# Kernel optimization log

Hardware: AMD Instinct MI355X
Metric: run time of the kernel (lower is better)

Reference implementation:

```python
import jax, jax.numpy as jnp
import numpy as np

N_HEAD = 16
D_MODEL = 1024
D_K = 64
D_V = 64
LN_EPS = 1e-5


def setup_inputs() -> dict:
    key = jax.random.key(0)
    ks = jax.random.split(key, 12)
    B, S = 4, 1024
    std_qkv = np.sqrt(2.0 / (D_MODEL + D_K)).astype(np.float32)
    inp = {
        "q": jax.random.normal(ks[0], (B, S, D_MODEL), jnp.float32),
        "k": jax.random.normal(ks[1], (B, S, D_MODEL), jnp.float32),
        "v": jax.random.normal(ks[2], (B, S, D_MODEL), jnp.float32),
        "Wq": jax.random.normal(ks[3], (N_HEAD * D_K, D_MODEL), jnp.float32) * std_qkv,
        "bq": jnp.zeros((N_HEAD * D_K,), jnp.float32),
        "Wk": jax.random.normal(ks[4], (N_HEAD * D_K, D_MODEL), jnp.float32) * std_qkv,
        "bk": jnp.zeros((N_HEAD * D_K,), jnp.float32),
        "Wv": jax.random.normal(ks[5], (N_HEAD * D_K, D_MODEL), jnp.float32) * std_qkv,
        "bv": jnp.zeros((N_HEAD * D_K,), jnp.float32),
        "Wfc": jax.random.normal(ks[6], (D_MODEL, N_HEAD * D_V), jnp.float32) * np.sqrt(2.0 / (D_MODEL + N_HEAD * D_V)).astype(np.float32),
        "bfc": jnp.zeros((D_MODEL,), jnp.float32),
        "gamma": jnp.ones((D_MODEL,), jnp.float32),
        "beta": jnp.zeros((D_MODEL,), jnp.float32),
    }
    return inp


def reference(q, k, v, Wq, bq, Wk, bk, Wv, bv, Wfc, bfc, gamma, beta):
    B, S, D = q.shape
    residual = q
    # projections -> [B, S, H, d] -> [B, H, S, d]
    qh = (q @ Wq.T + bq).reshape(B, S, N_HEAD, D_K).transpose(0, 2, 1, 3)
    kh = (k @ Wk.T + bk).reshape(B, S, N_HEAD, D_K).transpose(0, 2, 1, 3)
    vh = (v @ Wv.T + bv).reshape(B, S, N_HEAD, D_V).transpose(0, 2, 1, 3)
    # NOTE: faithful to source -- no 1/sqrt(d_k) scaling (temperature is None)
    scores = jnp.einsum('bhqd,bhkd->bhqk', qh, kh)  # [B, H, S, S]
    attn = jax.nn.softmax(scores, axis=-1)
    out = jnp.einsum('bhqk,bhkd->bhqd', attn, vh)  # [B, H, S, d_v]
    out = out.transpose(0, 2, 1, 3).reshape(B, S, N_HEAD * D_V)
    out = out @ Wfc.T + bfc  # dropout = identity at eval
    x = out + residual
    mu = jnp.mean(x, axis=-1, keepdims=True)
    var = jnp.var(x, axis=-1, keepdims=True)
    y = (x - mu) * jax.lax.rsqrt(var + LN_EPS) * gamma + beta
    # attn returned in source layout: (n_head*batch, S, S)
    attn_flat = attn.transpose(1, 0, 2, 3).reshape(N_HEAD * B, S, S)
    return (y, attn_flat)
```

## Files before the change

### kernel.cpp

```cpp
#include <hip/hip_runtime.h>
#include <stdint.h>

#define B_ 4
#define S_ 1024
#define D_ 1024
#define H_ 16
#define DK_ 64

typedef unsigned short u16;
typedef unsigned int   u32;
typedef short bf16x8 __attribute__((ext_vector_type(8)));
typedef float f32x4  __attribute__((ext_vector_type(4)));

__device__ __forceinline__ u16 f2bf(float x) {
    u32 u = __float_as_uint(x);
    return (u16)((u + 0x7fffu + ((u >> 16) & 1u)) >> 16);
}
__device__ __forceinline__ float bf2f(u16 h) {
    return __uint_as_float(((u32)h) << 16);
}

template <int OMODE, int AMODE>
__global__ __launch_bounds__(256) void gemm_mfma(const void* __restrict__ Ain,
                                                 const float* __restrict__ W,
                                                 const float* __restrict__ bias,
                                                 float* __restrict__ Cf,
                                                 u16* __restrict__ Chi,
                                                 u16* __restrict__ Clo,
                                                 int M, int N, int K) {
    __shared__ __align__(16) u16 AhS[128][40];
    __shared__ __align__(16) u16 AlS[128][40];
    __shared__ __align__(16) u16 WhS[128][40];
    __shared__ __align__(16) u16 WlS[128][40];

    const int t    = threadIdx.x;
    const int m0   = blockIdx.y * 128;
    const int n0   = blockIdx.x * 128;
    const int srow = t >> 1;
    const int sk   = (t & 1) * 16;
    const int w    = t >> 6;
    const int lane = t & 63;
    const int wr   = w >> 1, wc = w & 1;
    const int fr   = lane & 15;
    const int kg   = lane >> 4;

    const float* Af = (const float*)Ain;
    const u16*   Ab = (const u16*)Ain;

    const float* Wbase = W + (size_t)(n0 + srow) * K + sk;
    float4 pw[4];
#pragma unroll
    for (int i = 0; i < 4; ++i) pw[i] = *(const float4*)(Wbase + i * 4);

    float4 pa[4];
    uint4  ua[2];
    if constexpr (AMODE == 0) {
        const float* Abase = Af + (size_t)(m0 + srow) * K + sk;
#pragma unroll
        for (int i = 0; i < 4; ++i) pa[i] = *(const float4*)(Abase + i * 4);
    } else {
        const u16* Abase = Ab + (size_t)(m0 + srow) * K + sk;
        ua[0] = *(const uint4*)(Abase);
        ua[1] = *(const uint4*)(Abase + 8);
    }

    f32x4 acc[4][4] = {};

    for (int kc = 0; kc < K; kc += 32) {
        if constexpr (AMODE == 0) {
            u32 hA[8], lA[8];
#pragma unroll
            for (int i = 0; i < 4; ++i) {
                float xs[4] = {pa[i].x, pa[i].y, pa[i].z, pa[i].w};
#pragma unroll
                for (int j = 0; j < 2; ++j) {
                    u16 a0 = f2bf(xs[2 * j]), a1 = f2bf(xs[2 * j + 1]);
                    hA[i * 2 + j] = (u32)a0 | ((u32)a1 << 16);
                    lA[i * 2 + j] = (u32)f2bf(xs[2 * j] - bf2f(a0)) |
                                    ((u32)f2bf(xs[2 * j + 1] - bf2f(a1)) << 16);
                }
            }
            *(uint4*)&AhS[srow][sk]     = make_uint4(hA[0], hA[1], hA[2], hA[3]);
            *(uint4*)&AhS[srow][sk + 8] = make_uint4(hA[4], hA[5], hA[6], hA[7]);
            *(uint4*)&AlS[srow][sk]     = make_uint4(lA[0], lA[1], lA[2], lA[3]);
            *(uint4*)&AlS[srow][sk + 8] = make_uint4(lA[4], lA[5], lA[6], lA[7]);
        } else {
            *(uint4*)&AhS[srow][sk]     = ua[0];
            *(uint4*)&AhS[srow][sk + 8] = ua[1];
        }
        {
            u32 hW[8], lW[8];
#pragma unroll
            for (int i = 0; i < 4; ++i) {
                float ys[4] = {pw[i].x, pw[i].y, pw[i].z, pw[i].w};
#pragma unroll
                for (int j = 0; j < 2; ++j) {
                    u16 w0 = f2bf(ys[2 * j]), w1 = f2bf(ys[2 * j + 1]);
                    hW[i * 2 + j] = (u32)w0 | ((u32)w1 << 16);
                    lW[i * 2 + j] = (u32)f2bf(ys[2 * j] - bf2f(w0)) |
                                    ((u32)f2bf(ys[2 * j + 1] - bf2f(w1)) << 16);
                }
            }
            *(uint4*)&WhS[srow][sk]     = make_uint4(hW[0], hW[1], hW[2], hW[3]);
            *(uint4*)&WhS[srow][sk + 8] = make_uint4(hW[4], hW[5], hW[6], hW[7]);
            *(uint4*)&WlS[srow][sk]     = make_uint4(lW[0], lW[1], lW[2], lW[3]);
            *(uint4*)&WlS[srow][sk + 8] = make_uint4(lW[4], lW[5], lW[6], lW[7]);
        }
        __syncthreads();

        if (kc + 32 < K) {
            if constexpr (AMODE == 0) {
                const float* Abase = Af + (size_t)(m0 + srow) * K + sk;
#pragma unroll
                for (int i = 0; i < 4; ++i)
                    pa[i] = *(const float4*)(Abase + kc + 32 + i * 4);
            } else {
                const u16* Abase = Ab + (size_t)(m0 + srow) * K + sk;
                ua[0] = *(const uint4*)(Abase + kc + 32);
                ua[1] = *(const uint4*)(Abase + kc + 32 + 8);
            }
#pragma unroll
            for (int i = 0; i < 4; ++i)
                pw[i] = *(const float4*)(Wbase + kc + 32 + i * 4);
        }

        bf16x8 fah[4], fal[4], fwh[4], fwl[4];
#pragma unroll
        for (int mt = 0; mt < 4; ++mt) {
            fah[mt] = *(const bf16x8*)&AhS[wr * 64 + mt * 16 + fr][kg * 8];
            if constexpr (AMODE == 0)
                fal[mt] = *(const bf16x8*)&AlS[wr * 64 + mt * 16 + fr][kg * 8];
        }
#pragma unroll
        for (int nt = 0; nt < 4; ++nt) {
            fwh[nt] = *(const bf16x8*)&WhS[wc * 64 + nt * 16 + fr][kg * 8];
            fwl[nt] = *(const bf16x8*)&WlS[wc * 64 + nt * 16 + fr][kg * 8];
        }
#pragma unroll
        for (int mt = 0; mt < 4; ++mt)
#pragma unroll
            for (int nt = 0; nt < 4; ++nt) {
                acc[mt][nt] = __builtin_amdgcn_mfma_f32_16x16x32_bf16(
                    fah[mt], fwh[nt], acc[mt][nt], 0, 0, 0);
                acc[mt][nt] = __builtin_amdgcn_mfma_f32_16x16x32_bf16(
                    fah[mt], fwl[nt], acc[mt][nt], 0, 0, 0);
                if constexpr (AMODE == 0)
                    acc[mt][nt] = __builtin_amdgcn_mfma_f32_16x16x32_bf16(
                        fal[mt], fwh[nt], acc[mt][nt], 0, 0, 0);
            }
        __syncthreads();
    }

#pragma unroll
    for (int nt = 0; nt < 4; ++nt) {
        const int n  = n0 + wc * 64 + nt * 16 + fr;
        const float bn = bias[n];
#pragma unroll
        for (int mt = 0; mt < 4; ++mt) {
#pragma unroll
            for (int r = 0; r < 4; ++r) {
                const int m = m0 + wr * 64 + mt * 16 + kg * 4 + r;
                const float v = acc[mt][nt][r] + bn;
                if (OMODE == 0) {
                    Cf[(size_t)m * N + n] = v;
                } else {
                    const int b = m >> 10, s = m & (S_ - 1);
                    const int h = n >> 6, d = n & 63;
                    if (OMODE == 1) {
                        const size_t off = (((size_t)b * H_ + h) * S_ + s) * DK_ + d;
                        const u16 hh = f2bf(v);
                        Chi[off] = hh;
                        Clo[off] = f2bf(v - bf2f(hh));
                    } else {
                        Chi[(((size_t)b * H_ + h) * DK_ + d) * S_ + s] = f2bf(v);
                    }
                }
            }
        }
    }
}

__global__ __launch_bounds__(256) void fused_attn(const u16* __restrict__ Qhi,
                                                  const u16* __restrict__ Qlo,
                                                  const u16* __restrict__ Khi,
                                                  const u16* __restrict__ Klo,
                                                  const u16* __restrict__ VT,
                                                  float* __restrict__ attn,
                                                  u16* __restrict__ ctx) {
    const int bh = blockIdx.y;
    const int b  = bh >> 4, h = bh & 15;
    const int i0 = blockIdx.x * 32;
    const int t  = threadIdx.x;
    const int w  = t >> 6;
    const int lane = t & 63;
    const int c  = lane & 15;
    const int q  = lane >> 4;

    __shared__ __align__(16) u16 smem[2 * 128 * 64];
    u16* KhiL = smem;
    u16* KloL = smem + 128 * 64;
    u16* Pl   = smem;
    u16* VTl  = smem + 32 * 128;
    __shared__ float redS[4][32];

    bf16x8 qh[2][2], ql[2][2];
#pragma unroll
    for (int mt = 0; mt < 2; ++mt)
#pragma unroll
        for (int kf = 0; kf < 2; ++kf) {
            const size_t off = ((size_t)bh * S_ + i0 + mt * 16 + c) * DK_ + kf * 32 + q * 8;
            qh[mt][kf] = *(const bf16x8*)(Qhi + off);
            ql[mt][kf] = *(const bf16x8*)(Qlo + off);
        }

    f32x4 acc[2][16] = {};

#pragma unroll
    for (int ch = 0; ch < 8; ++ch) {
        __syncthreads();
#pragma unroll
        for (int u = 0; u < 4; ++u) {
            const int unit = t * 4 + u;
            const int j = unit >> 3, k16 = unit & 7;
            const int dstb = j * 128 + ((k16 * 16) ^ ((j & 7) << 4));
            const size_t src = ((size_t)bh * S_ + ch * 128 + j) * DK_ + k16 * 8;
            *(uint4*)((char*)KhiL + dstb) = *(const uint4*)(Khi + src);
            *(uint4*)((char*)KloL + dstb) = *(const uint4*)(Klo + src);
        }
        __syncthreads();
#pragma unroll
        for (int ct = 0; ct < 2; ++ct) {
            const int j = w * 32 + ct * 16 + c;
#pragma unroll
            for (int kf = 0; kf < 2; ++kf) {
                const int byt = j * 128 + ((kf * 64 + q * 16) ^ ((j & 7) << 4));
                bf16x8 kh = *(const bf16x8*)((char*)KhiL + byt);
                bf16x8 kl = *(const bf16x8*)((char*)KloL + byt);
#pragma unroll
                for (int mt = 0; mt < 2; ++mt) {
                    acc[mt][ch * 2 + ct] = __builtin_amdgcn_mfma_f32_16x16x32_bf16(
                        qh[mt][kf], kh, acc[mt][ch * 2 + ct], 0, 0, 0);
                    acc[mt][ch * 2 + ct] = __builtin_amdgcn_mfma_f32_16x16x32_bf16(
                        ql[mt][kf], kh, acc[mt][ch * 2 + ct], 0, 0, 0);
                    acc[mt][ch * 2 + ct] = __builtin_amdgcn_mfma_f32_16x16x32_bf16(
                        qh[mt][kf], kl, acc[mt][ch * 2 + ct], 0, 0, 0);
                }
            }
        }
    }

    float mx[2][4];
#pragma unroll
    for (int mt = 0; mt < 2; ++mt)
#pragma unroll
        for (int r = 0; r < 4; ++r) {
            float m = -1e30f;
#pragma unroll
            for (int ci = 0; ci < 16; ++ci) m = fmaxf(m, acc[mt][ci][r]);
#pragma unroll
            for (int o = 1; o < 16; o <<= 1) m = fmaxf(m, __shfl_xor(m, o, 64));
            mx[mt][r] = m;
        }
    if (c == 0) {
#pragma unroll
        for (int mt = 0; mt < 2; ++mt)
#pragma unroll
            for (int r = 0; r < 4; ++r) redS[w][mt * 16 + q * 4 + r] = mx[mt][r];
    }
    __syncthreads();
#pragma unroll
    for (int mt = 0; mt < 2; ++mt)
#pragma unroll
        for (int r = 0; r < 4; ++r) {
            const int row = mt * 16 + q * 4 + r;
            mx[mt][r] = fmaxf(fmaxf(redS[0][row], redS[1][row]),
                              fmaxf(redS[2][row], redS[3][row]));
        }
    float sm[2][4] = {};
#pragma unroll
    for (int mt = 0; mt < 2; ++mt)
#pragma unroll
        for (int ci = 0; ci < 16; ++ci)
#pragma unroll
            for (int r = 0; r < 4; ++r) {
                const float e = __expf(acc[mt][ci][r] - mx[mt][r]);
                acc[mt][ci][r] = e;
                sm[mt][r] += e;
            }
#pragma unroll
    for (int mt = 0; mt < 2; ++mt)
#pragma unroll
        for (int r = 0; r < 4; ++r)
#pragma unroll
            for (int o = 1; o < 16; o <<= 1) sm[mt][r] += __shfl_xor(sm[mt][r], o, 64);
    __syncthreads();
    if (c == 0) {
#pragma unroll
        for (int mt = 0; mt < 2; ++mt)
#pragma unroll
            for (int r = 0; r < 4; ++r) redS[w][mt * 16 + q * 4 + r] = sm[mt][r];
    }
    __syncthreads();
    float inv[2][4];
#pragma unroll
    for (int mt = 0; mt < 2; ++mt)
#pragma unroll
        for (int r = 0; r < 4; ++r) {
            const int row = mt * 16 + q * 4 + r;
            inv[mt][r] = 1.0f / (redS[0][row] + redS[1][row] + redS[2][row] + redS[3][row]);
        }
    float* dst = attn + ((size_t)(h * B_ + b) * S_ + i0) * S_;
#pragma unroll
    for (int mt = 0; mt < 2; ++mt)
#pragma unroll
        for (int ci = 0; ci < 16; ++ci)
#pragma unroll
            for (int r = 0; r < 4; ++r) {
                const float p = acc[mt][ci][r] * inv[mt][r];
                acc[mt][ci][r] = p;
                const int row = mt * 16 + q * 4 + r;
                const int col = (ci >> 1) * 128 + w * 32 + (ci & 1) * 16 + c;
                dst[(size_t)row * S_ + col] = p;
            }

    f32x4 c2[2] = {};
#pragma unroll
    for (int ch = 0; ch < 8; ++ch) {
        __syncthreads();
#pragma unroll
        for (int mt = 0; mt < 2; ++mt)
#pragma unroll
            for (int ct = 0; ct < 2; ++ct)
#pragma unroll
                for (int r = 0; r < 4; ++r) {
                    const int row = mt * 16 + q * 4 + r;
                    const int col = w * 32 + ct * 16 + c;
                    const int byt = row * 256 + ((col * 2) ^ ((row & 7) << 4));
                    *(u16*)((char*)Pl + byt) = f2bf(acc[mt][ch * 2 + ct][r]);
                }
#pragma unroll
        for (int u = 0; u < 4; ++u) {
            const int unit = t * 4 + u;
            const int d = unit >> 4, s16 = unit & 15;
            const int byt = d * 256 + ((s16 * 16) ^ ((d & 7) << 4));
            *(uint4*)((char*)VTl + byt) =
                *(const uint4*)(VT + ((size_t)bh * DK_ + d) * S_ + ch * 128 + s16 * 8);
        }
        __syncthreads();
#pragma unroll
        for (int kf = 0; kf < 4; ++kf) {
            const int dloc = w * 16 + c;
            const int vb_byt = dloc * 256 + ((kf * 64 + q * 16) ^ ((c & 7) << 4));
            bf16x8 vb = *(const bf16x8*)((char*)VTl + vb_byt);
#pragma unroll
            for (int mt = 0; mt < 2; ++mt) {
                const int pr = mt * 16 + c;
                const int pa_byt = pr * 256 + ((kf * 64 + q * 16) ^ ((c & 7) << 4));
                bf16x8 pa = *(const bf16x8*)((char*)Pl + pa_byt);
                c2[mt] = __builtin_amdgcn_mfma_f32_16x16x32_bf16(pa, vb, c2[mt], 0, 0, 0);
            }
        }
    }
#pragma unroll
    for (int mt = 0; mt < 2; ++mt)
#pragma unroll
        for (int r = 0; r < 4; ++r) {
            const int s = i0 + mt * 16 + q * 4 + r;
            ctx[((size_t)b * S_ + s) * D_ + h * DK_ + w * 16 + c] = f2bf(c2[mt][r]);
        }
}

__global__ __launch_bounds__(256) void ln_kernel(const float* __restrict__ X,
                                                 const float* __restrict__ q,
                                                 const float* __restrict__ gamma,
                                                 const float* __restrict__ beta,
                                                 float* __restrict__ y) {
    const int row = blockIdx.x;
    const int t   = threadIdx.x;
    const size_t base = (size_t)row * D_;

    float4 xv = *(const float4*)(X + base + t * 4);
    float4 qv = *(const float4*)(q + base + t * 4);
    const float x0 = xv.x + qv.x, x1 = xv.y + qv.y;
    const float x2 = xv.z + qv.z, x3 = xv.w + qv.w;

    float sum = x0 + x1 + x2 + x3;
    float sq  = x0 * x0 + x1 * x1 + x2 * x2 + x3 * x3;
#pragma unroll
    for (int o = 32; o > 0; o >>= 1) {
        sum += __shfl_xor(sum, o, 64);
        sq  += __shfl_xor(sq, o, 64);
    }
    __shared__ float red[8];
    const int wv = t >> 6;
    if ((t & 63) == 0) { red[wv] = sum; red[4 + wv] = sq; }
    __syncthreads();
    sum = red[0] + red[1] + red[2] + red[3];
    sq  = red[4] + red[5] + red[6] + red[7];

    const float mu  = sum * (1.0f / 1024.0f);
    const float var = sq * (1.0f / 1024.0f) - mu * mu;
    const float rs  = rsqrtf(var + 1e-5f);

    float4 gv = *(const float4*)(gamma + t * 4);
    float4 bv = *(const float4*)(beta + t * 4);
    float4 o;
    o.x = (x0 - mu) * rs * gv.x + bv.x;
    o.y = (x1 - mu) * rs * gv.y + bv.y;
    o.z = (x2 - mu) * rs * gv.z + bv.z;
    o.w = (x3 - mu) * rs * gv.w + bv.w;
    *(float4*)(y + base + t * 4) = o;
}

extern "C" void kernel_launch(void* const* d_in, const int* in_sizes, int n_in,
                              void* d_out, int out_size, void* d_ws, size_t ws_size,
                              hipStream_t stream) {
    const float* q    = (const float*)d_in[0];
    const float* k    = (const float*)d_in[1];
    const float* v    = (const float*)d_in[2];
    const float* Wq   = (const float*)d_in[3];
    const float* bq   = (const float*)d_in[4];
    const float* Wk   = (const float*)d_in[5];
    const float* bk   = (const float*)d_in[6];
    const float* Wv   = (const float*)d_in[7];
    const float* bv   = (const float*)d_in[8];
    const float* Wfc  = (const float*)d_in[9];
    const float* bfc  = (const float*)d_in[10];
    const float* gamma= (const float*)d_in[11];
    const float* beta = (const float*)d_in[12];

    float* y_out    = (float*)d_out;
    float* attn_out = (float*)d_out + (size_t)B_ * S_ * D_;

    float* ws   = (float*)d_ws;
    u16*  Qhi   = (u16*)(ws);
    u16*  Qlo   = (u16*)(ws + 2097152);
    u16*  Khi   = (u16*)(ws + 4194304);
    u16*  Klo   = (u16*)(ws + 6291456);
    u16*  VTb   = (u16*)(ws + 8388608);
    u16*  ctxb  = (u16*)(ws + 10485760);
    float* xbuf = ws;

    const dim3 gg(8, 32), bb(256);
    gemm_mfma<1, 0><<<gg, bb, 0, stream>>>(q, Wq, bq, nullptr, Qhi, Qlo, 4096, 1024, 1024);
    gemm_mfma<1, 0><<<gg, bb, 0, stream>>>(k, Wk, bk, nullptr, Khi, Klo, 4096, 1024, 1024);
    gemm_mfma<2, 0><<<gg, bb, 0, stream>>>(v, Wv, bv, nullptr, VTb, nullptr, 4096, 1024, 1024);

    fused_attn<<<dim3(32, 64), bb, 0, stream>>>(Qhi, Qlo, Khi, Klo, VTb, attn_out, ctxb);

    gemm_mfma<0, 1><<<gg, bb, 0, stream>>>(ctxb, Wfc, bfc, xbuf, nullptr, nullptr, 4096, 1024, 1024);
    ln_kernel<<<4096, 256, 0, stream>>>(xbuf, q, gamma, beta, y_out);
}
```

Baseline: 694.3 us.

## Remove LDS staging and barriers from attention, split PV by key chunk

The fused attention kernel now loads K hi/lo fragments straight from global memory into registers instead of staging them in LDS behind per-chunk barriers. The P·V stage is repartitioned so each wave multiplies its own 32-key slice of P, written to a private double-buffered LDS area, against V read directly from global memory. The four partial context tiles are then summed through LDS with a single barrier. Occupancy is hinted at two blocks per CU. This removes most __syncthreads calls in exchange for more global/L2 traffic for K and V, an extra cross-wave reduction, and higher register pressure.

```diff
diff --git a/kernel.cpp b/kernel.cpp
--- a/kernel.cpp
+++ b/kernel.cpp
@@ -180,13 +180,13 @@
     }
 }
 
-__global__ __launch_bounds__(256) void fused_attn(const u16* __restrict__ Qhi,
-                                                  const u16* __restrict__ Qlo,
-                                                  const u16* __restrict__ Khi,
-                                                  const u16* __restrict__ Klo,
-                                                  const u16* __restrict__ VT,
-                                                  float* __restrict__ attn,
-                                                  u16* __restrict__ ctx) {
+__global__ __launch_bounds__(256, 2) void fused_attn(const u16* __restrict__ Qhi,
+                                                     const u16* __restrict__ Qlo,
+                                                     const u16* __restrict__ Khi,
+                                                     const u16* __restrict__ Klo,
+                                                     const u16* __restrict__ VT,
+                                                     float* __restrict__ attn,
+                                                     u16* __restrict__ ctx) {
     const int bh = blockIdx.y;
     const int b  = bh >> 4, h = bh & 15;
     const int i0 = blockIdx.x * 32;
@@ -196,11 +196,7 @@
     const int c  = lane & 15;
     const int q  = lane >> 4;
 
-    __shared__ __align__(16) u16 smem[2 * 128 * 64];
-    u16* KhiL = smem;
-    u16* KloL = smem + 128 * 64;
-    u16* Pl   = smem;
-    u16* VTl  = smem + 32 * 128;
+    __shared__ __align__(16) float pf[4][32][64];
     __shared__ float redS[4][32];
 
     bf16x8 qh[2][2], ql[2][2];
@@ -213,29 +209,21 @@
             ql[mt][kf] = *(const bf16x8*)(Qlo + off);
         }
 
+    const u16* Kh_g = Khi + (size_t)bh * S_ * DK_;
+    const u16* Kl_g = Klo + (size_t)bh * S_ * DK_;
+
     f32x4 acc[2][16] = {};
 
 #pragma unroll
     for (int ch = 0; ch < 8; ++ch) {
-        __syncthreads();
-#pragma unroll
-        for (int u = 0; u < 4; ++u) {
-            const int unit = t * 4 + u;
-            const int j = unit >> 3, k16 = unit & 7;
-            const int dstb = j * 128 + ((k16 * 16) ^ ((j & 7) << 4));
-            const size_t src = ((size_t)bh * S_ + ch * 128 + j) * DK_ + k16 * 8;
-            *(uint4*)((char*)KhiL + dstb) = *(const uint4*)(Khi + src);
-            *(uint4*)((char*)KloL + dstb) = *(const uint4*)(Klo + src);
-        }
-        __syncthreads();
 #pragma unroll
         for (int ct = 0; ct < 2; ++ct) {
-            const int j = w * 32 + ct * 16 + c;
+            const int j = ch * 128 + w * 32 + ct * 16 + c;
 #pragma unroll
             for (int kf = 0; kf < 2; ++kf) {
-                const int byt = j * 128 + ((kf * 64 + q * 16) ^ ((j & 7) << 4));
-                bf16x8 kh = *(const bf16x8*)((char*)KhiL + byt);
-                bf16x8 kl = *(const bf16x8*)((char*)KloL + byt);
+                const size_t ko = (size_t)j * DK_ + kf * 32 + q * 8;
+                bf16x8 kh = *(const bf16x8*)(Kh_g + ko);
+                bf16x8 kl = *(const bf16x8*)(Kl_g + ko);
 #pragma unroll
                 for (int mt = 0; mt < 2; ++mt) {
                     acc[mt][ch * 2 + ct] = __builtin_amdgcn_mfma_f32_16x16x32_bf16(
@@ -323,51 +311,68 @@
                 dst[(size_t)row * S_ + col] = p;
             }
 
-    f32x4 c2[2] = {};
+    const u16* VT_g = VT + (size_t)bh * DK_ * S_;
+    u16* swb = (u16*)&pf[w][0][0];
+    f32x4 ctxa[2][4] = {};
+
 #pragma unroll
     for (int ch = 0; ch < 8; ++ch) {
-        __syncthreads();
+        u16* sw = swb + (ch & 1) * 2048;
 #pragma unroll
         for (int mt = 0; mt < 2; ++mt)
 #pragma unroll
-            for (int ct = 0; ct < 2; ++ct)
+            for (int ctl = 0; ctl < 2; ++ctl)
 #pragma unroll
                 for (int r = 0; r < 4; ++r) {
                     const int row = mt * 16 + q * 4 + r;
-                    const int col = w * 32 + ct * 16 + c;
-                    const int byt = row * 256 + ((col * 2) ^ ((row & 7) << 4));
-                    *(u16*)((char*)Pl + byt) = f2bf(acc[mt][ch * 2 + ct][r]);
+                    const int col = ctl * 16 + c;
+                    const int byt = row * 64 + ((col * 2) ^ (((row >> 1) & 3) << 4));
+                    *(u16*)((char*)sw + byt) = f2bf(acc[mt][ch * 2 + ctl][r]);
                 }
-#pragma unroll
-        for (int u = 0; u < 4; ++u) {
-            const int unit = t * 4 + u;
-            const int d = unit >> 4, s16 = unit & 15;
-            const int byt = d * 256 + ((s16 * 16) ^ ((d & 7) << 4));
-            *(uint4*)((char*)VTl + byt) =
-                *(const uint4*)(VT + ((size_t)bh * DK_ + d) * S_ + ch * 128 + s16 * 8);
-        }
-        __syncthreads();
-#pragma unroll
-        for (int kf = 0; kf < 4; ++kf) {
-            const int dloc = w * 16 + c;
-            const int vb_byt = dloc * 256 + ((kf * 64 + q * 16) ^ ((c & 7) << 4));
-            bf16x8 vb = *(const bf16x8*)((char*)VTl + vb_byt);
-#pragma unroll
-            for (int mt = 0; mt < 2; ++mt) {
-                const int pr = mt * 16 + c;
-                const int pa_byt = pr * 256 + ((kf * 64 + q * 16) ^ ((c & 7) << 4));
-                bf16x8 pa = *(const bf16x8*)((char*)Pl + pa_byt);
-                c2[mt] = __builtin_amdgcn_mfma_f32_16x16x32_bf16(pa, vb, c2[mt], 0, 0, 0);
-            }
-        }
-    }
-#pragma unroll
-    for (int mt = 0; mt < 2; ++mt)
-#pragma unroll
-        for (int r = 0; r < 4; ++r) {
-            const int s = i0 + mt * 16 + q * 4 + r;
-            ctx[((size_t)b * S_ + s) * D_ + h * DK_ + w * 16 + c] = f2bf(c2[mt][r]);
-        }
+        bf16x8 pa[2];
+#pragma unroll
+        for (int mt = 0; mt < 2; ++mt) {
+            const int row = mt * 16 + c;
+            const int byt = row * 64 + ((q * 16) ^ (((row >> 1) & 3) << 4));
+            pa[mt] = *(const bf16x8*)((char*)sw + byt);
+        }
+#pragma unroll
+        for (int dt = 0; dt < 4; ++dt) {
+            const int d = dt * 16 + c;
+            bf16x8 vb = *(const bf16x8*)(VT_g + (size_t)d * S_ + ch * 128 + w * 32 + q * 8);
+#pragma unroll
+            for (int mt = 0; mt < 2; ++mt)
+                ctxa[mt][dt] = __builtin_amdgcn_mfma_f32_16x16x32_bf16(
+                    pa[mt], vb, ctxa[mt][dt], 0, 0, 0);
+        }
+    }
+
+#pragma unroll
+    for (int mt = 0; mt < 2; ++mt)
+#pragma unroll
+        for (int dt = 0; dt < 4; ++dt)
+#pragma unroll
+            for (int r = 0; r < 4; ++r)
+                pf[w][mt * 16 + q * 4 + r][dt * 16 + c] = ctxa[mt][dt][r];
+    __syncthreads();
+
+    {
+        const int rrow = t >> 3, d0 = (t & 7) * 8;
+        float s[8] = {};
+#pragma unroll
+        for (int ww = 0; ww < 4; ++ww) {
+            float4 a0 = *(const float4*)&pf[ww][rrow][d0];
+            float4 a1 = *(const float4*)&pf[ww][rrow][d0 + 4];
+            s[0] += a0.x; s[1] += a0.y; s[2] += a0.z; s[3] += a0.w;
+            s[4] += a1.x; s[5] += a1.y; s[6] += a1.z; s[7] += a1.w;
+        }
+        u32 p0 = (u32)f2bf(s[0]) | ((u32)f2bf(s[1]) << 16);
+        u32 p1 = (u32)f2bf(s[2]) | ((u32)f2bf(s[3]) << 16);
+        u32 p2 = (u32)f2bf(s[4]) | ((u32)f2bf(s[5]) << 16);
+        u32 p3 = (u32)f2bf(s[6]) | ((u32)f2bf(s[7]) << 16);
+        *(uint4*)(ctx + ((size_t)b * S_ + i0 + rrow) * D_ + h * DK_ + d0) =
+            make_uint4(p0, p1, p2, p3);
+    }
 }
 
 __global__ __launch_bounds__(256) void ln_kernel(const float* __restrict__ X,
```

Result: faster. 661.5 us (-4.7%).
